# Performance work log

Hardware: AMD Instinct MI355X
Metric: run time of the kernel (lower is better)

The kernel has to match this reference:

```python
import jax, jax.numpy as jnp
import numpy as np
import math

B, S, D = 1, 1024, 4096
H, HD, KVH = 32, 128, 8
R, FF = 16, 14336
EPS = 1e-5


def setup_inputs() -> dict:
    key = jax.random.key(0)
    ks = jax.random.split(key, 32)
    def nrm(i, shape, scale):
        return jax.random.normal(ks[i], shape, dtype=jnp.float32) * scale
    inp = {}
    inp["x"] = nrm(0, (B, S, D), 0.5)
    inp["norm_w1"] = jnp.ones((D,), jnp.float32)
    inp["norm_w2"] = jnp.ones((D,), jnp.float32)
    # rotary embedding tables (Mistral theta=10000)
    inv_freq = 1.0 / (10000.0 ** (jnp.arange(0, HD, 2, dtype=jnp.float32) / HD))
    freqs = jnp.outer(jnp.arange(S, dtype=jnp.float32), inv_freq)
    emb = jnp.concatenate([freqs, freqs], axis=-1)  # [S, HD]
    inp["cos"] = jnp.cos(emb)
    inp["sin"] = jnp.sin(emb)
    causal = jnp.tril(jnp.ones((S, S), dtype=bool))
    inp["mask"] = jnp.where(causal, 0.0, -1e9).astype(jnp.float32)[None, None]  # [1,1,S,S]
    w_shapes = {"wq": (D, D), "wk": (KVH * HD, D), "wv": (KVH * HD, D),
                "wo": (D, D), "wg": (FF, D), "wu": (FF, D), "wd": (D, FF)}
    i = 1
    for name, shp in w_shapes.items():
        inp[name] = nrm(i, shp, 0.02); i += 1
        dout, din = shp
        inp["la_" + name[1]] = nrm(i, (din, R), 0.02); i += 1
        inp["lb_" + name[1]] = nrm(i, (R, dout), 0.02); i += 1
    inp["num_heads"] = H
    inp["head_dim"] = HD
    inp["num_kv_heads"] = KVH
    return inp


def _rms(x, w):
    # rmsnorm_forward with eps=1e-5, weight only
    return x * jax.lax.rsqrt(jnp.mean(x * x, axis=-1, keepdims=True) + EPS) * w


def _lora(x, W, la, lb):
    # dequantized base weight [out,in] applied as x @ W.T, plus low-rank delta
    return x @ W.T + (x @ la) @ lb


def _rope(x, cos, sin):
    # x: [B, h, S, HD]; rotate_half convention
    x1, x2 = jnp.split(x, 2, axis=-1)
    rot = jnp.concatenate([-x2, x1], axis=-1)
    return x * cos[None, None] + rot * sin[None, None]


def _layer(x, norm_w1, norm_w2, cos, sin, mask,
           wq, la_q, lb_q, wk, la_k, lb_k, wv, la_v, lb_v, wo, la_o, lb_o,
           wg, la_g, lb_g, wu, la_u, lb_u, wd, la_d, lb_d,
           num_heads, head_dim, num_kv_heads):
    b, s, d = x.shape
    n_rep = num_heads // num_kv_heads
    xn1 = _rms(x, norm_w1)
    q = _lora(xn1, wq, la_q, lb_q).reshape(b, s, num_heads, head_dim).transpose(0, 2, 1, 3)
    k = _lora(xn1, wk, la_k, lb_k).reshape(b, s, num_kv_heads, head_dim).transpose(0, 2, 1, 3)
    v = _lora(xn1, wv, la_v, lb_v).reshape(b, s, num_kv_heads, head_dim).transpose(0, 2, 1, 3)
    q = _rope(q, cos, sin)
    k = _rope(k, cos, sin)
    k = jnp.repeat(k, n_rep, axis=1)
    v = jnp.repeat(v, n_rep, axis=1)
    scores = jnp.einsum("bhqd,bhkd->bhqk", q, k) / math.sqrt(head_dim) + mask
    a = jax.nn.softmax(scores, axis=-1)
    o = jnp.einsum("bhqk,bhkd->bhqd", a, v).transpose(0, 2, 1, 3).reshape(b, s, d)
    o = _lora(o, wo, la_o, lb_o)
    x_med = x + o
    xn2 = _rms(x_med, norm_w2)
    gate = _lora(xn2, wg, la_g, lb_g)
    up = _lora(xn2, wu, la_u, lb_u)
    h = jax.nn.silu(gate) * up
    down = _lora(h, wd, la_d, lb_d)
    return x_med + down


def reference(x, norm_w1, norm_w2, cos, sin, mask,
              wq, la_q, lb_q, wk, la_k, lb_k, wv, la_v, lb_v, wo, la_o, lb_o,
              wg, la_g, lb_g, wu, la_u, lb_u, wd, la_d, lb_d,
              num_heads, head_dim, num_kv_heads):
    return _layer(x, norm_w1, norm_w2, cos, sin, mask,
                  wq, la_q, lb_q, wk, la_k, lb_k, wv, la_v, lb_v, wo, la_o, lb_o,
                  wg, la_g, lb_g, wu, la_u, lb_u, wd, la_d, lb_d,
                  num_heads, head_dim, num_kv_heads)
```

## Files before the change

### kernel.cpp

```cpp
#include <hip/hip_runtime.h>
#include <hip/hip_bf16.h>
#include <math.h>

#define SEQ 1024
#define DIM 4096
#define NH 32
#define HD 128
#define NKVH 8
#define FF 14336
#define LR 16

typedef __attribute__((ext_vector_type(8))) short bf16x8;
typedef __attribute__((ext_vector_type(4))) float f32x4;
typedef __attribute__((ext_vector_type(4))) ushort ushort4v;
typedef __attribute__((ext_vector_type(4))) unsigned int u32x4;

__device__ __forceinline__ ushort f2bf(float f) {
  union { float f; unsigned u; } v; v.f = f;
  unsigned r = (v.u + 0x7FFFu + ((v.u >> 16) & 1u)) >> 16;
  return (ushort)r;
}
__device__ __forceinline__ float bf2f(ushort h) {
  union { unsigned u; float f; } v; v.u = ((unsigned)h) << 16;
  return v.f;
}
__device__ __forceinline__ unsigned cvtpk(float a, float b) {
  unsigned r;
  asm("v_cvt_pk_bf16_f32 %0, %1, %2" : "=v"(r) : "v"(a), "v"(b));
  return r;
}

__device__ __forceinline__ void gload_lds16(const void* g, void* l) {
  __builtin_amdgcn_global_load_lds(
      (const __attribute__((address_space(1))) void*)g,
      (__attribute__((address_space(3))) void*)l, 16, 0, 0);
}

__global__ __launch_bounds__(256) void rmsnorm_kernel(const float* __restrict__ x,
                                                      const float* __restrict__ w,
                                                      ushort* __restrict__ out) {
  int row = blockIdx.x;
  int tid = threadIdx.x;
  const float* xr = x + (size_t)row * DIM;
  float vals[16];
  float s = 0.f;
#pragma unroll
  for (int c = 0; c < 4; c++) {
    float4 v = *(const float4*)&xr[(tid + c * 256) * 4];
    vals[c * 4 + 0] = v.x; vals[c * 4 + 1] = v.y;
    vals[c * 4 + 2] = v.z; vals[c * 4 + 3] = v.w;
    s += v.x * v.x + v.y * v.y + v.z * v.z + v.w * v.w;
  }
#pragma unroll
  for (int off = 32; off >= 1; off >>= 1) s += __shfl_down(s, off);
  __shared__ float wsum[4];
  __shared__ float scale_s;
  int lane = tid & 63, wv = tid >> 6;
  if (lane == 0) wsum[wv] = s;
  __syncthreads();
  if (tid == 0) {
    float t = wsum[0] + wsum[1] + wsum[2] + wsum[3];
    scale_s = rsqrtf(t / (float)DIM + 1e-5f);
  }
  __syncthreads();
  float scale = scale_s;
  ushort* orow = out + (size_t)row * DIM;
#pragma unroll
  for (int c = 0; c < 4; c++) {
    int base = (tid + c * 256) * 4;
    float4 wv4 = *(const float4*)&w[base];
    ushort4v ov;
    ov.x = f2bf(vals[c * 4 + 0] * scale * wv4.x);
    ov.y = f2bf(vals[c * 4 + 1] * scale * wv4.y);
    ov.z = f2bf(vals[c * 4 + 2] * scale * wv4.z);
    ov.w = f2bf(vals[c * 4 + 3] * scale * wv4.w);
    *(ushort4v*)&orow[base] = ov;
  }
}

template <int NL>
__global__ __launch_bounds__(256) void lora_a_kernel(
    const ushort* __restrict__ A,
    const float* __restrict__ la0, const float* __restrict__ la1,
    const float* __restrict__ la2,
    ushort* __restrict__ t0, ushort* __restrict__ t1, ushort* __restrict__ t2,
    int K) {
  int m = blockIdx.x, i = threadIdx.x;
  float acc[NL][16];
#pragma unroll
  for (int l = 0; l < NL; l++)
#pragma unroll
    for (int n = 0; n < 16; n++) acc[l][n] = 0.f;

  const ushort* Arow = A + (size_t)m * K;
  int nc = K >> 8;
  for (int c = 0; c < nc; c++) {
    int k = c * 256 + i;
    float a = bf2f(Arow[k]);
#pragma unroll
    for (int l = 0; l < NL; l++) {
      const float* lap = (l == 0 ? la0 : (l == 1 ? la1 : la2)) + (size_t)k * 16;
#pragma unroll
      for (int q = 0; q < 4; q++) {
        float4 lv = *(const float4*)&lap[q * 4];
        acc[l][q * 4 + 0] += a * lv.x;
        acc[l][q * 4 + 1] += a * lv.y;
        acc[l][q * 4 + 2] += a * lv.z;
        acc[l][q * 4 + 3] += a * lv.w;
      }
    }
  }

  __shared__ float red[256][17];
  __shared__ float red2[16][17];
#pragma unroll
  for (int l = 0; l < NL; l++) {
    __syncthreads();
#pragma unroll
    for (int n = 0; n < 16; n++) red[i][n] = acc[l][n];
    __syncthreads();
    {
      int g = i >> 4, n = i & 15;
      float s = 0.f;
#pragma unroll
      for (int j = 0; j < 16; j++) s += red[g * 16 + j][n];
      red2[g][n] = s;
    }
    __syncthreads();
    if (i < 16) {
      float s2 = 0.f;
#pragma unroll
      for (int g2 = 0; g2 < 16; g2++) s2 += red2[g2][i];
      ushort* tp = (l == 0 ? t0 : (l == 1 ? t1 : t2));
      tp[(size_t)m * LR + i] = f2bf(s2);
    }
  }
}

template <int WM>
__global__ __launch_bounds__(512) void gemm256_kernel(
    const ushort* __restrict__ A,
    const float* __restrict__ W0, const float* __restrict__ W1, const float* __restrict__ W2,
    const float* __restrict__ lb0, const float* __restrict__ lb1, const float* __restrict__ lb2,
    const ushort* __restrict__ t0, const ushort* __restrict__ t1, const ushort* __restrict__ t2,
    const ushort* __restrict__ gatep,
    int c1, int c2, void* __restrict__ outp, int M, int N, int K, int nkp) {
  __shared__ __align__(16) ushort As[2][256 * 64];
  __shared__ __align__(16) ushort Bs[2][256 * 64];
  int tid = threadIdx.x;
  int lane = tid & 63, wave = tid >> 6;
  int wm = wave >> 2, wn = wave & 3;

  int gx = gridDim.x, gy = gridDim.y, gz = gridDim.z;
  int flat = blockIdx.x + gx * (blockIdx.y + gy * blockIdx.z);
  int nwg = gx * gy * gz;
  int q = nwg >> 3, r = nwg & 7;
  int xcd = flat & 7;
  int wgid = (xcd < r ? xcd * (q + 1) : r * (q + 1) + (xcd - r) * q) + (flat >> 3);
  int sh = gy * gz;
  int bx = wgid / sh;
  int rem = wgid - bx * sh;
  int z = rem / gy;
  int by = rem - z * gy;

  int n0 = bx * 256, m0 = by * 256;
  int k0 = z * nkp;

  const float* Wp; const float* lbp; const ushort* tp; int nseg, wseg;
  if (n0 < c1)      { Wp = W0; lbp = lb0; tp = t0; nseg = n0;      wseg = c1; }
  else if (n0 < c2) { Wp = W1; lbp = lb1; tp = t1; nseg = n0 - c1; wseg = c2 - c1; }
  else              { Wp = W2; lbp = lb2; tp = t2; nseg = n0 - c2; wseg = N - c2; }

  int srow = tid >> 3;
  int sswz = ((tid & 7) ^ (srow & 7)) * 8;
  const ushort* Ab = A + (size_t)(m0 + srow) * K + sswz;
  const float* Wbase = Wp + (size_t)(nseg + srow) * K + (tid & 7) * 8;

  f32x4 acc[8][4] = {};
  float4 breg[8];

#define SHALF(kt, b, h)                                                       \
  _Pragma("unroll") for (int i = 2 * (h); i < 2 * (h) + 2; i++) {             \
    gload_lds16(Ab + (size_t)(i * 64) * K + (size_t)(kt) * 64,                \
                &As[b][wave * 512 + i * 4096]);                               \
  }
#define BLOAD(kt, h)                                                          \
  {                                                                           \
    const float* gp = Wbase + (size_t)((h) * 128) * K + (size_t)(kt) * 64;    \
    breg[(h) * 4 + 0] = *(const float4*)gp;                                   \
    breg[(h) * 4 + 1] = *(const float4*)(gp + 4);                             \
    breg[(h) * 4 + 2] = *(const float4*)(gp + (size_t)64 * K);                \
    breg[(h) * 4 + 3] = *(const float4*)(gp + (size_t)64 * K + 4);            \
  }
#define WRITE_B(b)                                                            \
  _Pragma("unroll") for (int h = 0; h < 2; h++)                               \
  _Pragma("unroll") for (int j = 0; j < 2; j++) {                             \
    int rr = h * 128 + j * 64 + srow;                                         \
    float4 lo = breg[h * 4 + j * 2 + 0];                                      \
    float4 hi = breg[h * 4 + j * 2 + 1];                                      \
    u32x4 v;                                                                  \
    v.x = cvtpk(lo.x, lo.y); v.y = cvtpk(lo.z, lo.w);                         \
    v.z = cvtpk(hi.x, hi.y); v.w = cvtpk(hi.z, hi.w);                         \
    *(u32x4*)&Bs[b][rr * 64 + (((tid & 7) ^ (rr & 7))) * 8] = v;              \
  }
#define LDFRAG(buf, rr, ks) \
  (*(const bf16x8*)&(buf)[(rr) * 64 + (((ks) * 4 + (lane >> 4)) ^ ((rr) & 7)) * 8])

  BLOAD(k0, 0); BLOAD(k0, 1);
  SHALF(k0, 0, 0); SHALF(k0, 0, 1);
  asm volatile("s_waitcnt vmcnt(4)" ::: "memory");
  WRITE_B(0);
  if (nkp > 1) { BLOAD(k0 + 1, 0); BLOAD(k0 + 1, 1); }
  if (nkp > 1) asm volatile("s_waitcnt vmcnt(8)" ::: "memory");
  else         asm volatile("s_waitcnt vmcnt(0)" ::: "memory");
  asm volatile("s_waitcnt lgkmcnt(0)" ::: "memory");
  __builtin_amdgcn_s_barrier();
  __builtin_amdgcn_sched_barrier(0);

  for (int tau = 0; tau < nkp; tau++) {
    int b = tau & 1;
    bool s1 = (tau + 1 < nkp), s2 = (tau + 2 < nkp);
    const ushort* as = As[b];
    const ushort* bs = Bs[b];
    bf16x8 bfr[4][2];
#pragma unroll
    for (int p = 0; p < 4; p++) {
      bf16x8 af[2][2];
#pragma unroll
      for (int qq = 0; qq < 2; qq++) {
        int ra = wm * 128 + (p * 2 + qq) * 16 + (lane & 15);
#pragma unroll
        for (int ks = 0; ks < 2; ks++) af[qq][ks] = LDFRAG(as, ra, ks);
      }
      if (p == 0) {
#pragma unroll
        for (int f = 0; f < 4; f++) {
          int rb = wn * 64 + f * 16 + (lane & 15);
#pragma unroll
          for (int ks = 0; ks < 2; ks++) bfr[f][ks] = LDFRAG(bs, rb, ks);
        }
      }
      if (p == 0 && s1) { SHALF(k0 + tau + 1, b ^ 1, 0); }
      if (p == 1 && s1) { SHALF(k0 + tau + 1, b ^ 1, 1); }
      if (p == 2 && s2) { BLOAD(k0 + tau + 2, 0); }
      if (p == 3 && s2) { BLOAD(k0 + tau + 2, 1); }
      __builtin_amdgcn_sched_barrier(0);
      __builtin_amdgcn_s_barrier();
      asm volatile("s_waitcnt lgkmcnt(0)" ::: "memory");
      __builtin_amdgcn_sched_barrier(0);
      __builtin_amdgcn_s_setprio(1);
#pragma unroll
      for (int qq = 0; qq < 2; qq++)
#pragma unroll
        for (int fn = 0; fn < 4; fn++)
#pragma unroll
          for (int ks = 0; ks < 2; ks++)
            acc[p * 2 + qq][fn] = __builtin_amdgcn_mfma_f32_16x16x32_bf16(
                af[qq][ks], bfr[fn][ks], acc[p * 2 + qq][fn], 0, 0, 0);
      __builtin_amdgcn_s_setprio(0);
      __builtin_amdgcn_sched_barrier(0);
      if (p == 1 && s1) {
        asm volatile("s_waitcnt vmcnt(4)" ::: "memory");
        WRITE_B(b ^ 1);
        __builtin_amdgcn_sched_barrier(0);
      }
      if (p == 3) {
        if (s2) asm volatile("s_waitcnt vmcnt(8)" ::: "memory");
        else    asm volatile("s_waitcnt vmcnt(0)" ::: "memory");
      }
      __builtin_amdgcn_s_barrier();
      __builtin_amdgcn_sched_barrier(0);
    }
  }
#undef SHALF
#undef BLOAD
#undef WRITE_B

  if (z == 0) {
#pragma unroll
    for (int it = 0; it < 2; it++) {
      int task = tid + it * 512;
      int rr = task >> 2, ls = task & 3;
      int ph = ls ^ (rr & 7);
      bf16x8 avv = {};
      bf16x8 bvv = {};
      if (ls < 2) {
        avv = *(const bf16x8*)&tp[(size_t)(m0 + rr) * LR + ls * 8];
#pragma unroll
        for (int j = 0; j < 8; j++)
          bvv[j] = (short)f2bf(lbp[(size_t)(ls * 8 + j) * wseg + nseg + rr]);
      }
      *(bf16x8*)&As[0][rr * 64 + ph * 8] = avv;
      *(bf16x8*)&Bs[0][rr * 64 + ph * 8] = bvv;
    }
    __syncthreads();
    bf16x8 af[8], bfr[4];
#pragma unroll
    for (int f = 0; f < 8; f++) {
      int ra = wm * 128 + f * 16 + (lane & 15);
      af[f] = LDFRAG(As[0], ra, 0);
    }
#pragma unroll
    for (int f = 0; f < 4; f++) {
      int rb = wn * 64 + f * 16 + (lane & 15);
      bfr[f] = LDFRAG(Bs[0], rb, 0);
    }
#pragma unroll
    for (int fm = 0; fm < 8; fm++)
#pragma unroll
      for (int fn = 0; fn < 4; fn++)
        acc[fm][fn] = __builtin_amdgcn_mfma_f32_16x16x32_bf16(af[fm], bfr[fn], acc[fm][fn], 0, 0, 0);
  }
#undef LDFRAG

#pragma unroll
  for (int fm = 0; fm < 8; fm++) {
#pragma unroll
    for (int j = 0; j < 4; j++) {
      int mg = m0 + wm * 128 + fm * 16 + (lane >> 4) * 4 + j;
#pragma unroll
      for (int fn = 0; fn < 4; fn++) {
        int ng = n0 + wn * 64 + fn * 16 + (lane & 15);
        float v = acc[fm][fn][j];
        if (WM == 0) {
          ((ushort*)outp)[(size_t)mg * N + ng] = f2bf(v);
        } else if (WM == 4) {
          float g = bf2f(gatep[(size_t)mg * N + ng]);
          float sv = g / (1.f + __expf(-g));
          ((ushort*)outp)[(size_t)mg * N + ng] = f2bf(sv * v);
        } else {
          ((float*)outp)[((size_t)z * M + mg) * (size_t)N + ng] = v;
        }
      }
    }
  }
}

__global__ __launch_bounds__(256) void reduce2_qkv_rope(const float* __restrict__ p,
                                                        const float* __restrict__ ct,
                                                        const float* __restrict__ st,
                                                        ushort* __restrict__ qb,
                                                        ushort* __restrict__ kb,
                                                        ushort* __restrict__ vtb) {
  int gidx = blockIdx.x * 256 + threadIdx.x;
  int r = gidx / 896, j = gidx - r * 896;
  size_t row = (size_t)r * 6144;
  size_t sstride = (size_t)SEQ * 6144;
  if (j < 640) {
    bool isq = j < 512;
    int jj = isq ? j : j - 512;
    int h = jj >> 4, d0 = (jj & 15) * 4;
    size_t base = row + (isq ? 0 : DIM) + h * 128 + d0;
    float4 a1 = *(const float4*)&p[base];
    float4 b1 = *(const float4*)&p[base + sstride];
    float4 a2 = *(const float4*)&p[base + 64];
    float4 b2 = *(const float4*)&p[base + 64 + sstride];
    float4 x1, x2;
    x1.x = a1.x + b1.x; x1.y = a1.y + b1.y; x1.z = a1.z + b1.z; x1.w = a1.w + b1.w;
    x2.x = a2.x + b2.x; x2.y = a2.y + b2.y; x2.z = a2.z + b2.z; x2.w = a2.w + b2.w;
    float4 c = *(const float4*)&ct[r * HD + d0];
    float4 s = *(const float4*)&st[r * HD + d0];
    float sc = isq ? 0.08838834764831845f : 1.0f;
    ushort4v o1, o2;
    o1.x = f2bf((x1.x * c.x - x2.x * s.x) * sc);
    o1.y = f2bf((x1.y * c.y - x2.y * s.y) * sc);
    o1.z = f2bf((x1.z * c.z - x2.z * s.z) * sc);
    o1.w = f2bf((x1.w * c.w - x2.w * s.w) * sc);
    o2.x = f2bf((x2.x * c.x + x1.x * s.x) * sc);
    o2.y = f2bf((x2.y * c.y + x1.y * s.y) * sc);
    o2.z = f2bf((x2.z * c.z + x1.z * s.z) * sc);
    o2.w = f2bf((x2.w * c.w + x1.w * s.w) * sc);
    if (isq) {
      *(ushort4v*)&qb[(size_t)r * DIM + h * 128 + d0] = o1;
      *(ushort4v*)&qb[(size_t)r * DIM + h * 128 + d0 + 64] = o2;
    } else {
      *(ushort4v*)&kb[(size_t)r * 1024 + h * 128 + d0] = o1;
      *(ushort4v*)&kb[(size_t)r * 1024 + h * 128 + d0 + 64] = o2;
    }
  } else {
    int jj = j - 640;
    int c0 = jj * 4;
    size_t base = row + DIM + 1024 + c0;
    float4 a = *(const float4*)&p[base];
    float4 b = *(const float4*)&p[base + sstride];
    vtb[(size_t)(c0 + 0) * SEQ + r] = f2bf(a.x + b.x);
    vtb[(size_t)(c0 + 1) * SEQ + r] = f2bf(a.y + b.y);
    vtb[(size_t)(c0 + 2) * SEQ + r] = f2bf(a.z + b.z);
    vtb[(size_t)(c0 + 3) * SEQ + r] = f2bf(a.w + b.w);
  }
}

__global__ __launch_bounds__(256) void reduce4_res_kernel(const float* __restrict__ p,
                                                          const float* __restrict__ res,
                                                          float* __restrict__ out,
                                                          size_t sstride) {
  size_t i = ((size_t)blockIdx.x * 256 + threadIdx.x) * 4;
  float4 a = *(const float4*)&p[i];
  float4 b = *(const float4*)&p[i + sstride];
  float4 c = *(const float4*)&p[i + 2 * sstride];
  float4 d = *(const float4*)&p[i + 3 * sstride];
  float4 r = *(const float4*)&res[i];
  float4 o;
  o.x = a.x + b.x + c.x + d.x + r.x;
  o.y = a.y + b.y + c.y + d.y + r.y;
  o.z = a.z + b.z + c.z + d.z + r.z;
  o.w = a.w + b.w + c.w + d.w + r.w;
  *(float4*)&out[i] = o;
}

__global__ __launch_bounds__(256) void reduce4_res_rms(const float* __restrict__ p,
                                                       const float* __restrict__ res,
                                                       const float* __restrict__ w,
                                                       float* __restrict__ xmed,
                                                       ushort* __restrict__ xn2,
                                                       size_t sstride) {
  int row = blockIdx.x, tid = threadIdx.x;
  size_t base = (size_t)row * DIM;
  float vals[16];
  float sq = 0.f;
#pragma unroll
  for (int c = 0; c < 4; c++) {
    size_t i = base + (tid + c * 256) * 4;
    float4 a = *(const float4*)&p[i];
    float4 b = *(const float4*)&p[i + sstride];
    float4 cc = *(const float4*)&p[i + 2 * sstride];
    float4 d = *(const float4*)&p[i + 3 * sstride];
    float4 r = *(const float4*)&res[i];
    float4 v;
    v.x = a.x + b.x + cc.x + d.x + r.x;
    v.y = a.y + b.y + cc.y + d.y + r.y;
    v.z = a.z + b.z + cc.z + d.z + r.z;
    v.w = a.w + b.w + cc.w + d.w + r.w;
    *(float4*)&xmed[i] = v;
    vals[c * 4 + 0] = v.x; vals[c * 4 + 1] = v.y;
    vals[c * 4 + 2] = v.z; vals[c * 4 + 3] = v.w;
    sq += v.x * v.x + v.y * v.y + v.z * v.z + v.w * v.w;
  }
#pragma unroll
  for (int off = 32; off >= 1; off >>= 1) sq += __shfl_down(sq, off);
  __shared__ float wsum[4];
  __shared__ float scale_s;
  int lane = tid & 63, wv = tid >> 6;
  if (lane == 0) wsum[wv] = sq;
  __syncthreads();
  if (tid == 0) {
    float t = wsum[0] + wsum[1] + wsum[2] + wsum[3];
    scale_s = rsqrtf(t / (float)DIM + 1e-5f);
  }
  __syncthreads();
  float scale = scale_s;
#pragma unroll
  for (int c = 0; c < 4; c++) {
    int off = (tid + c * 256) * 4;
    float4 wv4 = *(const float4*)&w[off];
    ushort4v ov;
    ov.x = f2bf(vals[c * 4 + 0] * scale * wv4.x);
    ov.y = f2bf(vals[c * 4 + 1] * scale * wv4.y);
    ov.z = f2bf(vals[c * 4 + 2] * scale * wv4.z);
    ov.w = f2bf(vals[c * 4 + 3] * scale * wv4.w);
    *(ushort4v*)&xn2[base + off] = ov;
  }
}

__global__ __launch_bounds__(256) void attn_kernel(const ushort* __restrict__ q,
                                                   const ushort* __restrict__ k,
                                                   const ushort* __restrict__ vt,
                                                   ushort* __restrict__ o) {
  int flat = blockIdx.x + 16 * blockIdx.y;
  int kvh = flat & 7;
  int idx = flat >> 3;
  int h = kvh * 4 + (idx & 3);
  int qb = idx >> 2;
  int tid = threadIdx.x, lane = tid & 63, wave = tid >> 6;
  __shared__ ushort Ks[64][136];
  __shared__ ushort Vs[128][72];
  __shared__ ushort Ps[4][16][72];

  bf16x8 qf[4];
  int qrow = qb * 64 + wave * 16 + (lane & 15);
#pragma unroll
  for (int kk = 0; kk < 4; kk++)
    qf[kk] = *(const bf16x8*)&q[(size_t)qrow * DIM + h * HD + kk * 32 + (lane >> 4) * 8];

  f32x4 oacc[8] = {};
  float mrow[4], lrow[4];
  int qr[4];
#pragma unroll
  for (int j = 0; j < 4; j++) {
    mrow[j] = -INFINITY; lrow[j] = 0.f;
    qr[j] = qb * 64 + wave * 16 + (lane >> 4) * 4 + j;
  }

  for (int kt = 0; kt <= qb; kt++) {
    int key0 = kt * 64;
#pragma unroll
    for (int c = 0; c < 4; c++) {
      int e = tid * 32 + c * 8;
      int r = e >> 7, cc = e & 127;
      *(bf16x8*)&Ks[r][cc] =
          *(const bf16x8*)&k[(size_t)(key0 + r) * (NKVH * HD) + kvh * HD + cc];
      int r2 = e >> 6, cc2 = e & 63;
      *(bf16x8*)&Vs[r2][cc2] =
          *(const bf16x8*)&vt[(size_t)(kvh * HD + r2) * SEQ + key0 + cc2];
    }
    __syncthreads();

    f32x4 sf[4] = {};
#pragma unroll
    for (int fn = 0; fn < 4; fn++)
#pragma unroll
      for (int kk = 0; kk < 4; kk++) {
        bf16x8 kf = *(const bf16x8*)&Ks[fn * 16 + (lane & 15)][kk * 32 + (lane >> 4) * 8];
        sf[fn] = __builtin_amdgcn_mfma_f32_16x16x32_bf16(qf[kk], kf, sf[fn], 0, 0, 0);
      }

#pragma unroll
    for (int fn = 0; fn < 4; fn++) {
      int key = key0 + fn * 16 + (lane & 15);
#pragma unroll
      for (int j = 0; j < 4; j++)
        if (key > qr[j]) sf[fn][j] = -INFINITY;
    }

#pragma unroll
    for (int j = 0; j < 4; j++) {
      float mx = fmaxf(fmaxf(sf[0][j], sf[1][j]), fmaxf(sf[2][j], sf[3][j]));
#pragma unroll
      for (int off = 1; off < 16; off <<= 1) mx = fmaxf(mx, __shfl_xor(mx, off));
      float mnew = fmaxf(mrow[j], mx);
      float sc = __expf(mrow[j] - mnew);
      mrow[j] = mnew;
      float rs = 0.f;
#pragma unroll
      for (int fn = 0; fn < 4; fn++) {
        float p = __expf(sf[fn][j] - mnew);
        sf[fn][j] = p;
        rs += p;
      }
#pragma unroll
      for (int off = 1; off < 16; off <<= 1) rs += __shfl_xor(rs, off);
      lrow[j] = lrow[j] * sc + rs;
#pragma unroll
      for (int f2 = 0; f2 < 8; f2++) oacc[f2][j] *= sc;
    }

#pragma unroll
    for (int fn = 0; fn < 4; fn++)
#pragma unroll
      for (int j = 0; j < 4; j++)
        Ps[wave][(lane >> 4) * 4 + j][fn * 16 + (lane & 15)] = f2bf(sf[fn][j]);

#pragma unroll
    for (int kk = 0; kk < 2; kk++) {
      bf16x8 pf = *(const bf16x8*)&Ps[wave][lane & 15][kk * 32 + (lane >> 4) * 8];
#pragma unroll
      for (int f2 = 0; f2 < 8; f2++) {
        bf16x8 vf = *(const bf16x8*)&Vs[f2 * 16 + (lane & 15)][kk * 32 + (lane >> 4) * 8];
        oacc[f2] = __builtin_amdgcn_mfma_f32_16x16x32_bf16(pf, vf, oacc[f2], 0, 0, 0);
      }
    }
    __syncthreads();
  }

#pragma unroll
  for (int j = 0; j < 4; j++) {
    float inv = 1.f / lrow[j];
#pragma unroll
    for (int f2 = 0; f2 < 8; f2++)
      o[(size_t)qr[j] * DIM + h * HD + f2 * 16 + (lane & 15)] = f2bf(oacc[f2][j] * inv);
  }
}

extern "C" void kernel_launch(void* const* d_in, const int* in_sizes, int n_in,
                              void* d_out, int out_size, void* d_ws, size_t ws_size,
                              hipStream_t stream) {
  const float* x    = (const float*)d_in[0];
  const float* w1   = (const float*)d_in[1];
  const float* w2   = (const float*)d_in[2];
  const float* cosT = (const float*)d_in[3];
  const float* sinT = (const float*)d_in[4];
  const float* wq = (const float*)d_in[6];
  const float* la_q = (const float*)d_in[7];
  const float* lb_q = (const float*)d_in[8];
  const float* wk = (const float*)d_in[9];
  const float* la_k = (const float*)d_in[10];
  const float* lb_k = (const float*)d_in[11];
  const float* wv = (const float*)d_in[12];
  const float* la_v = (const float*)d_in[13];
  const float* lb_v = (const float*)d_in[14];
  const float* wo = (const float*)d_in[15];
  const float* la_o = (const float*)d_in[16];
  const float* lb_o = (const float*)d_in[17];
  const float* wg = (const float*)d_in[18];
  const float* la_g = (const float*)d_in[19];
  const float* lb_g = (const float*)d_in[20];
  const float* wu = (const float*)d_in[21];
  const float* la_u = (const float*)d_in[22];
  const float* lb_u = (const float*)d_in[23];
  const float* wd = (const float*)d_in[24];
  const float* la_d = (const float*)d_in[25];
  const float* lb_d = (const float*)d_in[26];
  float* out = (float*)d_out;

  char* ws = (char*)d_ws;
  ushort* xn1 = (ushort*)ws;  ws += (size_t)SEQ * DIM * 2;
  ushort* qb  = (ushort*)ws;  ws += (size_t)SEQ * DIM * 2;
  ushort* kb  = (ushort*)ws;  ws += (size_t)SEQ * NKVH * HD * 2;
  ushort* vtb = (ushort*)ws;  ws += (size_t)SEQ * NKVH * HD * 2;
  ushort* ob  = (ushort*)ws;  ws += (size_t)SEQ * DIM * 2;
  float*  xmed= (float*)ws;   ws += (size_t)SEQ * DIM * 4;
  ushort* xn2 = (ushort*)ws;  ws += (size_t)SEQ * DIM * 2;
  ushort* gate= (ushort*)ws;  ws += (size_t)SEQ * FF * 2;
  ushort* up  = (ushort*)ws;  ws += (size_t)SEQ * FF * 2;
  ushort* hb  = (ushort*)ws;  ws += (size_t)SEQ * FF * 2;
  ushort* t_q = (ushort*)ws; ws += SEQ * LR * 2;
  ushort* t_k = (ushort*)ws; ws += SEQ * LR * 2;
  ushort* t_v = (ushort*)ws; ws += SEQ * LR * 2;
  ushort* t_o = (ushort*)ws; ws += SEQ * LR * 2;
  ushort* t_g = (ushort*)ws; ws += SEQ * LR * 2;
  ushort* t_u = (ushort*)ws; ws += SEQ * LR * 2;
  ushort* t_d = (ushort*)ws; ws += SEQ * LR * 2;
  (void)up;

  float* pbuf1 = (float*)gate;
  float* pbuf2 = (float*)xn2;

  size_t snd = (size_t)SEQ * DIM;

  rmsnorm_kernel<<<SEQ, 256, 0, stream>>>(x, w1, xn1);
  lora_a_kernel<3><<<SEQ, 256, 0, stream>>>(xn1, la_q, la_k, la_v, t_q, t_k, t_v, DIM);

  gemm256_kernel<3><<<dim3((DIM + 2048) / 256, SEQ / 256, 2), 512, 0, stream>>>(
      xn1, wq, wk, wv, lb_q, lb_k, lb_v, t_q, t_k, t_v, nullptr, DIM, DIM + 1024,
      pbuf1, SEQ, DIM + 2048, DIM, 32);
  reduce2_qkv_rope<<<SEQ * 896 / 256, 256, 0, stream>>>(pbuf1, cosT, sinT, qb, kb, vtb);

  attn_kernel<<<dim3(SEQ / 64, NH), 256, 0, stream>>>(qb, kb, vtb, ob);

  lora_a_kernel<1><<<SEQ, 256, 0, stream>>>(ob, la_o, la_o, la_o, t_o, t_o, t_o, DIM);
  gemm256_kernel<3><<<dim3(DIM / 256, SEQ / 256, 4), 512, 0, stream>>>(
      ob, wo, wo, wo, lb_o, lb_o, lb_o, t_o, t_o, t_o, nullptr, DIM, DIM,
      pbuf1, SEQ, DIM, DIM, 16);
  reduce4_res_rms<<<SEQ, 256, 0, stream>>>(pbuf1, x, w2, xmed, xn2, snd);

  lora_a_kernel<2><<<SEQ, 256, 0, stream>>>(xn2, la_g, la_u, la_u, t_g, t_u, t_u, DIM);
  gemm256_kernel<0><<<dim3(FF / 256, SEQ / 256, 1), 512, 0, stream>>>(
      xn2, wg, wg, wg, lb_g, lb_g, lb_g, t_g, t_g, t_g, nullptr, FF, FF,
      gate, SEQ, FF, DIM, DIM / 64);
  gemm256_kernel<4><<<dim3(FF / 256, SEQ / 256, 1), 512, 0, stream>>>(
      xn2, wu, wu, wu, lb_u, lb_u, lb_u, t_u, t_u, t_u, gate, FF, FF,
      hb, SEQ, FF, DIM, DIM / 64);
  lora_a_kernel<1><<<SEQ, 256, 0, stream>>>(hb, la_d, la_d, la_d, t_d, t_d, t_d, FF);
  gemm256_kernel<3><<<dim3(DIM / 256, SEQ / 256, 4), 512, 0, stream>>>(
      hb, wd, wd, wd, lb_d, lb_d, lb_d, t_d, t_d, t_d, nullptr, DIM, DIM,
      pbuf2, SEQ, DIM, FF, FF / 4 / 64);
  reduce4_res_kernel<<<snd / 1024, 256, 0, stream>>>(pbuf2, xmed, out, snd);
}
```

Baseline: 872.7 us.

## Deepen fp32 weight register prefetch to three tiles with double register sets

The fp32 weight tile register prefetch in the fused LoRA GEMM now runs three K-tiles ahead instead of two. It uses two alternating register buffers (even and odd) and unrolls the main K loop by two. The goal is to hide more global-load latency of the weight stream before the bf16 conversion and LDS write. In exchange it costs about 32 extra VGPRs, which could lower occupancy or cause spills. The unrolled loop also assumes an even number of K-tiles per split.

```diff
diff --git a/kernel.cpp b/kernel.cpp
--- a/kernel.cpp
+++ b/kernel.cpp
@@ -177,27 +177,27 @@
   const float* Wbase = Wp + (size_t)(nseg + srow) * K + (tid & 7) * 8;
 
   f32x4 acc[8][4] = {};
-  float4 breg[8];
+  float4 bregE[8], bregO[8];
 
 #define SHALF(kt, b, h)                                                       \
   _Pragma("unroll") for (int i = 2 * (h); i < 2 * (h) + 2; i++) {             \
     gload_lds16(Ab + (size_t)(i * 64) * K + (size_t)(kt) * 64,                \
                 &As[b][wave * 512 + i * 4096]);                               \
   }
-#define BLOAD(kt, h)                                                          \
+#define BLOADX(REG, kt, h)                                                    \
   {                                                                           \
     const float* gp = Wbase + (size_t)((h) * 128) * K + (size_t)(kt) * 64;    \
-    breg[(h) * 4 + 0] = *(const float4*)gp;                                   \
-    breg[(h) * 4 + 1] = *(const float4*)(gp + 4);                             \
-    breg[(h) * 4 + 2] = *(const float4*)(gp + (size_t)64 * K);                \
-    breg[(h) * 4 + 3] = *(const float4*)(gp + (size_t)64 * K + 4);            \
-  }
-#define WRITE_B(b)                                                            \
+    REG[(h) * 4 + 0] = *(const float4*)gp;                                    \
+    REG[(h) * 4 + 1] = *(const float4*)(gp + 4);                              \
+    REG[(h) * 4 + 2] = *(const float4*)(gp + (size_t)64 * K);                 \
+    REG[(h) * 4 + 3] = *(const float4*)(gp + (size_t)64 * K + 4);             \
+  }
+#define WRITE_BX(REG, b)                                                      \
   _Pragma("unroll") for (int h = 0; h < 2; h++)                               \
   _Pragma("unroll") for (int j = 0; j < 2; j++) {                             \
     int rr = h * 128 + j * 64 + srow;                                         \
-    float4 lo = breg[h * 4 + j * 2 + 0];                                      \
-    float4 hi = breg[h * 4 + j * 2 + 1];                                      \
+    float4 lo = REG[h * 4 + j * 2 + 0];                                       \
+    float4 hi = REG[h * 4 + j * 2 + 1];                                       \
     u32x4 v;                                                                  \
     v.x = cvtpk(lo.x, lo.y); v.y = cvtpk(lo.z, lo.w);                         \
     v.z = cvtpk(hi.x, hi.y); v.w = cvtpk(hi.z, hi.w);                         \
@@ -206,75 +206,80 @@
 #define LDFRAG(buf, rr, ks) \
   (*(const bf16x8*)&(buf)[(rr) * 64 + (((ks) * 4 + (lane >> 4)) ^ ((rr) & 7)) * 8])
 
-  BLOAD(k0, 0); BLOAD(k0, 1);
+#define TILE_BODY(b, TAU, CREG)                                               \
+  {                                                                           \
+    int tau_ = (TAU);                                                         \
+    bool s1_ = (tau_ + 1 < nkp);                                              \
+    bool s3_ = (tau_ + 3 < nkp);                                              \
+    const ushort* as_ = As[b];                                                \
+    const ushort* bs_ = Bs[b];                                                \
+    bf16x8 bfr[4][2];                                                         \
+    _Pragma("unroll") for (int p = 0; p < 4; p++) {                           \
+      bf16x8 af[2][2];                                                        \
+      _Pragma("unroll") for (int qq = 0; qq < 2; qq++) {                      \
+        int ra = wm * 128 + (p * 2 + qq) * 16 + (lane & 15);                  \
+        _Pragma("unroll") for (int ks = 0; ks < 2; ks++)                      \
+          af[qq][ks] = LDFRAG(as_, ra, ks);                                   \
+      }                                                                       \
+      if (p == 0) {                                                           \
+        _Pragma("unroll") for (int f = 0; f < 4; f++) {                       \
+          int rb = wn * 64 + f * 16 + (lane & 15);                            \
+          _Pragma("unroll") for (int ks = 0; ks < 2; ks++)                    \
+            bfr[f][ks] = LDFRAG(bs_, rb, ks);                                 \
+        }                                                                     \
+      }                                                                       \
+      if (p == 0 && s1_) { SHALF(k0 + tau_ + 1, (b) ^ 1, 0); }                \
+      if (p == 1 && s1_) { SHALF(k0 + tau_ + 1, (b) ^ 1, 1); }                \
+      if (p == 2 && s3_) { BLOADX(CREG, k0 + tau_ + 3, 0); }                  \
+      if (p == 3 && s3_) { BLOADX(CREG, k0 + tau_ + 3, 1); }                  \
+      __builtin_amdgcn_sched_barrier(0);                                      \
+      __builtin_amdgcn_s_barrier();                                           \
+      asm volatile("s_waitcnt lgkmcnt(0)" ::: "memory");                      \
+      __builtin_amdgcn_sched_barrier(0);                                      \
+      __builtin_amdgcn_s_setprio(1);                                          \
+      _Pragma("unroll") for (int qq = 0; qq < 2; qq++)                        \
+        _Pragma("unroll") for (int fn = 0; fn < 4; fn++)                      \
+          _Pragma("unroll") for (int ks = 0; ks < 2; ks++)                    \
+            acc[p * 2 + qq][fn] = __builtin_amdgcn_mfma_f32_16x16x32_bf16(    \
+                af[qq][ks], bfr[fn][ks], acc[p * 2 + qq][fn], 0, 0, 0);       \
+      __builtin_amdgcn_s_setprio(0);                                          \
+      __builtin_amdgcn_sched_barrier(0);                                      \
+      if (p == 1 && s1_) {                                                    \
+        if (s3_) asm volatile("s_waitcnt vmcnt(12)" ::: "memory");            \
+        else     asm volatile("s_waitcnt vmcnt(0)" ::: "memory");             \
+        WRITE_BX(CREG, (b) ^ 1);                                              \
+        __builtin_amdgcn_sched_barrier(0);                                    \
+      }                                                                       \
+      if (p == 3) {                                                           \
+        if (s3_) asm volatile("s_waitcnt vmcnt(16)" ::: "memory");            \
+        else     asm volatile("s_waitcnt vmcnt(0)" ::: "memory");             \
+      }                                                                       \
+      __builtin_amdgcn_s_barrier();                                           \
+      __builtin_amdgcn_sched_barrier(0);                                      \
+    }                                                                         \
+  }
+
+  BLOADX(bregE, k0, 0); BLOADX(bregE, k0, 1);
   SHALF(k0, 0, 0); SHALF(k0, 0, 1);
   asm volatile("s_waitcnt vmcnt(4)" ::: "memory");
-  WRITE_B(0);
-  if (nkp > 1) { BLOAD(k0 + 1, 0); BLOAD(k0 + 1, 1); }
-  if (nkp > 1) asm volatile("s_waitcnt vmcnt(8)" ::: "memory");
-  else         asm volatile("s_waitcnt vmcnt(0)" ::: "memory");
+  WRITE_BX(bregE, 0);
+  if (nkp > 1) { BLOADX(bregO, k0 + 1, 0); BLOADX(bregO, k0 + 1, 1); }
+  if (nkp > 2) { BLOADX(bregE, k0 + 2, 0); BLOADX(bregE, k0 + 2, 1); }
+  asm volatile("s_waitcnt vmcnt(16)" ::: "memory");
   asm volatile("s_waitcnt lgkmcnt(0)" ::: "memory");
   __builtin_amdgcn_s_barrier();
   __builtin_amdgcn_sched_barrier(0);
 
-  for (int tau = 0; tau < nkp; tau++) {
-    int b = tau & 1;
-    bool s1 = (tau + 1 < nkp), s2 = (tau + 2 < nkp);
-    const ushort* as = As[b];
-    const ushort* bs = Bs[b];
-    bf16x8 bfr[4][2];
-#pragma unroll
-    for (int p = 0; p < 4; p++) {
-      bf16x8 af[2][2];
-#pragma unroll
-      for (int qq = 0; qq < 2; qq++) {
-        int ra = wm * 128 + (p * 2 + qq) * 16 + (lane & 15);
-#pragma unroll
-        for (int ks = 0; ks < 2; ks++) af[qq][ks] = LDFRAG(as, ra, ks);
-      }
-      if (p == 0) {
-#pragma unroll
-        for (int f = 0; f < 4; f++) {
-          int rb = wn * 64 + f * 16 + (lane & 15);
-#pragma unroll
-          for (int ks = 0; ks < 2; ks++) bfr[f][ks] = LDFRAG(bs, rb, ks);
-        }
-      }
-      if (p == 0 && s1) { SHALF(k0 + tau + 1, b ^ 1, 0); }
-      if (p == 1 && s1) { SHALF(k0 + tau + 1, b ^ 1, 1); }
-      if (p == 2 && s2) { BLOAD(k0 + tau + 2, 0); }
-      if (p == 3 && s2) { BLOAD(k0 + tau + 2, 1); }
-      __builtin_amdgcn_sched_barrier(0);
-      __builtin_amdgcn_s_barrier();
-      asm volatile("s_waitcnt lgkmcnt(0)" ::: "memory");
-      __builtin_amdgcn_sched_barrier(0);
-      __builtin_amdgcn_s_setprio(1);
-#pragma unroll
-      for (int qq = 0; qq < 2; qq++)
-#pragma unroll
-        for (int fn = 0; fn < 4; fn++)
-#pragma unroll
-          for (int ks = 0; ks < 2; ks++)
-            acc[p * 2 + qq][fn] = __builtin_amdgcn_mfma_f32_16x16x32_bf16(
-                af[qq][ks], bfr[fn][ks], acc[p * 2 + qq][fn], 0, 0, 0);
-      __builtin_amdgcn_s_setprio(0);
-      __builtin_amdgcn_sched_barrier(0);
-      if (p == 1 && s1) {
-        asm volatile("s_waitcnt vmcnt(4)" ::: "memory");
-        WRITE_B(b ^ 1);
-        __builtin_amdgcn_sched_barrier(0);
-      }
-      if (p == 3) {
-        if (s2) asm volatile("s_waitcnt vmcnt(8)" ::: "memory");
-        else    asm volatile("s_waitcnt vmcnt(0)" ::: "memory");
-      }
-      __builtin_amdgcn_s_barrier();
-      __builtin_amdgcn_sched_barrier(0);
-    }
-  }
+  int nkp2 = nkp >> 1;
+  for (int t2 = 0; t2 < nkp2; t2++) {
+    int tau0 = 2 * t2;
+    TILE_BODY(0, tau0, bregO);
+    TILE_BODY(1, tau0 + 1, bregE);
+  }
+#undef TILE_BODY
 #undef SHALF
-#undef BLOAD
-#undef WRITE_B
+#undef BLOADX
+#undef WRITE_BX
 
   if (z == 0) {
 #pragma unroll
```

After: 945.8 us. 8.4% more time.
